# Performance work log

Measured on AMD Instinct MI355X. Metric: run time of the kernel, lower is better.

The kernel has to match this reference:

```python
import jax, jax.numpy as jnp
import numpy as np

LX = LY = KS = 14            # lengthX, lengthY, kernel_size
IN_BOND = 4
HID = 4                      # hidden_bond
CH = 2                       # channel
OUT = 10                     # output_dim
N = 32768                    # batch
LENGTH = LX * LY             # 196 sequential contraction steps
P = (LX - KS + 1) * (LY - KS + 1)  # number of patches (=1 here)
STD = 0.01
EPS = 1e-5                   # BatchNorm1d default eps


def setup_inputs() -> dict:
    key = jax.random.key(0)
    k0, k1, k2, k3 = jax.random.split(key, 4)
    x = jax.random.normal(k0, (N, IN_BOND, LX, LY), jnp.float32)
    # weights1[0]: [in_bond, hidden, channel]
    w_first = STD * jax.random.normal(k1, (IN_BOND, HID, CH), jnp.float32)
    # weights1[1..length-2]: [hidden, in_bond, hidden, channel], stacked
    w_mid = STD * jax.random.normal(k2, (LENGTH - 2, HID, IN_BOND, HID, CH), jnp.float32)
    # weights1[length-1]: [hidden, in_bond, output_dim, channel]
    w_last = STD * jax.random.normal(k3, (HID, IN_BOND, OUT, CH), jnp.float32)
    # shared BatchNorm1d(hidden) affine params
    gamma = jnp.ones((HID,), jnp.float32)
    beta = jnp.zeros((HID,), jnp.float32)
    return {"x": x, "w_first": w_first, "w_mid": w_mid, "w_last": w_last,
            "gamma": gamma, "beta": beta}


def reference(x, w_first, w_mid, w_last, gamma, beta):
    n = x.shape[0]
    # Patch extraction -> InputBucket [N, in_bond, KS*KS, P]
    buckets = []
    for k in range(LX - KS + 1):          # static, size 1 with defaults
        for l in range(LY - KS + 1):
            buckets.append(x[:, :, k:k + KS, l:l + KS].reshape(n, IN_BOND, KS * KS))
    ib = jnp.stack(buckets, axis=3)       # [N, in_bond, KS*KS, P]

    # Step 0: tensordot over in_bond, then permute -> y 'nbcr' = [N, P, CH, HID]
    y = jnp.einsum('nip,ihc->npch', ib[:, :, 0, :], w_first)

    # Middle steps 1..LENGTH-2 as a scan (strict sequential dependency chain)
    mids = jnp.moveaxis(ib[:, :, 1:LENGTH - 1, :], 2, 0)  # [LENGTH-2, N, in_bond, P]

    def step(y, inp):
        xi, w = inp  # xi: [N, in_bond, P]; w: [HID(r), IN_BOND(i), HID(h), CH(c)]
        # contra_w_d after permute: [N, P, CH, HID_left(r), HID_right(h)]
        contra = jnp.einsum('nip,rihc->npcrh', xi, w)
        y_new = jnp.einsum('npcr,npcrh->ncph', y, contra)  # 'ncbl': [N, CH, P, HID]
        # BatchNorm1d(HID) in training mode over flattened batch (biased var)
        flat = y_new.reshape(-1, HID)
        mean = jnp.mean(flat, axis=0)
        var = jnp.var(flat, axis=0)
        yb = (flat - mean) * jax.lax.rsqrt(var + EPS) * gamma + beta
        # faithful to torch's .view(-1, P, CH, HID) memory reinterpretation
        return yb.reshape(n, P, CH, HID), None

    y, _ = jax.lax.scan(step, y, (mids, w_mid))

    # Last step: -> [N, P, CH, HID, OUT] then einsum 'nbcr,nbcrl->nbcl'
    contra = jnp.einsum('nip,rioc->npcro', ib[:, :, LENGTH - 1, :], w_last)
    out = jnp.einsum('npcr,npcro->npco', y, contra)  # [N, P, CH, OUT]
    return out
```

## Files before the change

### kernel.cpp

```cpp
#include <hip/hip_runtime.h>

#define NSAMP 32768
#define INB   4
#define HIDN  4
#define CHN   2
#define OUTD  10
#define NPIX  196
#define NMID  194
#define BLK   256
#define SPT   2
#define NBLK  (NSAMP / (BLK * SPT))
#define INV_ROWS 1.52587890625e-05f
#define BN_EPS 1e-5f
#define SENT  0xFFFFFFFFFFFFFFFFull
#define WS_BYTES ((size_t)NMID * NBLK * 4 * sizeof(unsigned long long))

__device__ __forceinline__ float xcomp(const float4& v, int j) {
    return j == 0 ? v.x : j == 1 ? v.y : j == 2 ? v.z : v.w;
}

__device__ __forceinline__ void mid_step(
    int t, const float xv[SPT][INB], float y[SPT][CHN][HIDN],
    const float* __restrict__ wm,
    const float gm[HIDN], const float bt[HIDN],
    unsigned long long* __restrict__ slots,
    float (*pb)[8], float* totl, int tid)
{
    const float* w = wm + (long)t * (HIDN * INB * HIDN * CHN);
    float yn[SPT][CHN][HIDN];
#pragma unroll
    for (int s = 0; s < SPT; ++s)
#pragma unroll
        for (int c = 0; c < CHN; ++c)
#pragma unroll
            for (int h = 0; h < HIDN; ++h) yn[s][c][h] = 0.f;

#pragma unroll
    for (int s = 0; s < SPT; ++s)
#pragma unroll
        for (int r = 0; r < HIDN; ++r)
#pragma unroll
            for (int i = 0; i < INB; ++i) {
                float p0 = y[s][0][r] * xv[s][i];
                float p1 = y[s][1][r] * xv[s][i];
                const float* wri = w + r * (INB * HIDN * CHN) + i * (HIDN * CHN);
#pragma unroll
                for (int h = 0; h < HIDN; ++h) {
                    yn[s][0][h] = fmaf(p0, wri[h * CHN + 0], yn[s][0][h]);
                    yn[s][1][h] = fmaf(p1, wri[h * CHN + 1], yn[s][1][h]);
                }
            }
    float red[8];
#pragma unroll
    for (int h = 0; h < HIDN; ++h) {
        float sm = 0.f, sq = 0.f;
#pragma unroll
        for (int s = 0; s < SPT; ++s) {
            sm += yn[s][0][h] + yn[s][1][h];
            sq += yn[s][0][h] * yn[s][0][h] + yn[s][1][h] * yn[s][1][h];
        }
        red[h] = sm; red[4 + h] = sq;
    }
#pragma unroll
    for (int j = 0; j < 8; ++j)
#pragma unroll
        for (int off = 32; off > 0; off >>= 1)
            red[j] += __shfl_down(red[j], off);
    const int wv = tid >> 6, ln = tid & 63;
    if (ln == 0) {
#pragma unroll
        for (int j = 0; j < 8; ++j) pb[wv][j] = red[j];
    }
    __syncthreads();
    if (wv == 0) {
        if (ln < 4) {
            float lo = pb[0][2 * ln]     + pb[1][2 * ln]     + pb[2][2 * ln]     + pb[3][2 * ln];
            float hi = pb[0][2 * ln + 1] + pb[1][2 * ln + 1] + pb[2][2 * ln + 1] + pb[3][2 * ln + 1];
            unsigned long long v = ((unsigned long long)__float_as_uint(hi) << 32)
                                 |  (unsigned long long)__float_as_uint(lo);
            __hip_atomic_store(&slots[((size_t)t * NBLK + blockIdx.x) * 4 + ln], v,
                               __ATOMIC_RELAXED, __HIP_MEMORY_SCOPE_AGENT);
        }
        const unsigned long long* ps = &slots[((size_t)t * NBLK + ln) * 4];
        unsigned long long q0, q1, q2, q3;
        do {
            q0 = __hip_atomic_load(&ps[0], __ATOMIC_RELAXED, __HIP_MEMORY_SCOPE_AGENT);
            q1 = __hip_atomic_load(&ps[1], __ATOMIC_RELAXED, __HIP_MEMORY_SCOPE_AGENT);
            q2 = __hip_atomic_load(&ps[2], __ATOMIC_RELAXED, __HIP_MEMORY_SCOPE_AGENT);
            q3 = __hip_atomic_load(&ps[3], __ATOMIC_RELAXED, __HIP_MEMORY_SCOPE_AGENT);
        } while (!__all(q0 != SENT && q1 != SENT && q2 != SENT && q3 != SENT));
        float sm[8];
        sm[0] = __uint_as_float((unsigned)q0); sm[1] = __uint_as_float((unsigned)(q0 >> 32));
        sm[2] = __uint_as_float((unsigned)q1); sm[3] = __uint_as_float((unsigned)(q1 >> 32));
        sm[4] = __uint_as_float((unsigned)q2); sm[5] = __uint_as_float((unsigned)(q2 >> 32));
        sm[6] = __uint_as_float((unsigned)q3); sm[7] = __uint_as_float((unsigned)(q3 >> 32));
#pragma unroll
        for (int j = 0; j < 8; ++j)
#pragma unroll
            for (int off = 1; off < 64; off <<= 1)
                sm[j] += __shfl_xor(sm[j], off);
        if (ln < 8) totl[ln] = sm[ln];
    }
    __syncthreads();
    float sm[8];
#pragma unroll
    for (int j = 0; j < 8; ++j) sm[j] = totl[j];
#pragma unroll
    for (int h = 0; h < HIDN; ++h) {
        float m  = sm[h] * INV_ROWS;
        float v  = fmaf(-m, m, sm[4 + h] * INV_ROWS);
        float is = rsqrtf(v + BN_EPS) * gm[h];
        float sh = bt[h] - m * is;
#pragma unroll
        for (int s = 0; s < SPT; ++s) {
            y[s][0][h] = fmaf(yn[s][0][h], is, sh);
            y[s][1][h] = fmaf(yn[s][1][h], is, sh);
        }
    }
}

__global__ __launch_bounds__(BLK, 1)
void ttbn_main(const float* __restrict__ x,  const float* __restrict__ wf,
               const float* __restrict__ wm, const float* __restrict__ wl,
               const float* __restrict__ gamma, const float* __restrict__ beta,
               float* __restrict__ out, unsigned long long* __restrict__ slots)
{
    __shared__ float pb[BLK / 64][8];
    __shared__ float totl[8];
    const int tid = threadIdx.x;

    float gm[HIDN], bt[HIDN];
#pragma unroll
    for (int h = 0; h < HIDN; ++h) { gm[h] = gamma[h]; bt[h] = beta[h]; }

    const float* xn[SPT];
    long nidx[SPT];
#pragma unroll
    for (int s = 0; s < SPT; ++s) {
        nidx[s] = (long)blockIdx.x * (BLK * SPT) + s * BLK + tid;
        xn[s]   = x + nidx[s] * (INB * NPIX);
    }

    float4 xg[SPT][INB];
    float  y[SPT][CHN][HIDN];

#pragma unroll
    for (int s = 0; s < SPT; ++s)
#pragma unroll
        for (int i = 0; i < INB; ++i)
            xg[s][i] = *reinterpret_cast<const float4*>(xn[s] + i * NPIX);

#pragma unroll
    for (int s = 0; s < SPT; ++s)
#pragma unroll
        for (int c = 0; c < CHN; ++c)
#pragma unroll
            for (int h = 0; h < HIDN; ++h) {
                float acc = 0.f;
#pragma unroll
                for (int i = 0; i < INB; ++i)
                    acc = fmaf(xg[s][i].x, wf[i * (HIDN * CHN) + h * CHN + c], acc);
                y[s][c][h] = acc;
            }
#pragma unroll
    for (int slp = 1; slp < 4; ++slp) {
        float xv[SPT][INB];
#pragma unroll
        for (int s = 0; s < SPT; ++s)
#pragma unroll
            for (int i = 0; i < INB; ++i) xv[s][i] = xcomp(xg[s][i], slp);
        mid_step(slp - 1, xv, y, wm, gm, bt, slots, pb, totl, tid);
    }

#pragma unroll 1
    for (int g = 1; g < 48; ++g) {
#pragma unroll
        for (int s = 0; s < SPT; ++s)
#pragma unroll
            for (int i = 0; i < INB; ++i)
                xg[s][i] = *reinterpret_cast<const float4*>(xn[s] + i * NPIX + g * 4);
#pragma unroll
        for (int slp = 0; slp < 4; ++slp) {
            float xv[SPT][INB];
#pragma unroll
            for (int s = 0; s < SPT; ++s)
#pragma unroll
                for (int i = 0; i < INB; ++i) xv[s][i] = xcomp(xg[s][i], slp);
            mid_step(g * 4 + slp - 1, xv, y, wm, gm, bt, slots, pb, totl, tid);
        }
    }

#pragma unroll
    for (int s = 0; s < SPT; ++s)
#pragma unroll
        for (int i = 0; i < INB; ++i)
            xg[s][i] = *reinterpret_cast<const float4*>(xn[s] + i * NPIX + 192);
#pragma unroll
    for (int slp = 0; slp < 3; ++slp) {
        float xv[SPT][INB];
#pragma unroll
        for (int s = 0; s < SPT; ++s)
#pragma unroll
            for (int i = 0; i < INB; ++i) xv[s][i] = xcomp(xg[s][i], slp);
        mid_step(191 + slp, xv, y, wm, gm, bt, slots, pb, totl, tid);
    }
#pragma unroll
    for (int s = 0; s < SPT; ++s) {
        float xv[INB];
#pragma unroll
        for (int i = 0; i < INB; ++i) xv[i] = xg[s][i].w;
        float o0[OUTD], o1[OUTD];
#pragma unroll
        for (int od = 0; od < OUTD; ++od) { o0[od] = 0.f; o1[od] = 0.f; }
#pragma unroll
        for (int r = 0; r < 4; ++r)
#pragma unroll
            for (int i = 0; i < INB; ++i) {
                float p0 = y[s][0][r] * xv[i];
                float p1 = y[s][1][r] * xv[i];
                const float* wri = wl + r * (INB * OUTD * CHN) + i * (OUTD * CHN);
#pragma unroll
                for (int od = 0; od < OUTD; ++od) {
                    o0[od] = fmaf(p0, wri[od * CHN + 0], o0[od]);
                    o1[od] = fmaf(p1, wri[od * CHN + 1], o1[od]);
                }
            }
        float tmp[20];
#pragma unroll
        for (int od = 0; od < OUTD; ++od) { tmp[od] = o0[od]; tmp[10 + od] = o1[od]; }
        float4* o4 = reinterpret_cast<float4*>(out + nidx[s] * (CHN * OUTD));
#pragma unroll
        for (int q = 0; q < 5; ++q)
            o4[q] = make_float4(tmp[q * 4], tmp[q * 4 + 1], tmp[q * 4 + 2], tmp[q * 4 + 3]);
    }
}

extern "C" void kernel_launch(void* const* d_in, const int* in_sizes, int n_in,
                              void* d_out, int out_size, void* d_ws, size_t ws_size,
                              hipStream_t stream) {
    const float* x     = (const float*)d_in[0];
    const float* wf    = (const float*)d_in[1];
    const float* wm    = (const float*)d_in[2];
    const float* wl    = (const float*)d_in[3];
    const float* gamma = (const float*)d_in[4];
    const float* beta  = (const float*)d_in[5];
    float*       out   = (float*)d_out;
    unsigned long long* slots = (unsigned long long*)d_ws;

    hipMemsetAsync(d_ws, 0xFF, WS_BYTES, stream);

    void* args[] = { &x, &wf, &wm, &wl, &gamma, &beta, &out, &slots };
    hipLaunchCooperativeKernel((void*)ttbn_main, dim3(NBLK), dim3(BLK),
                               args, 0, stream);
}
```

Measured before the change: 848.7 us.

## Halve block count, simplify grid-wide BN reduction, prefetch inputs in float2 pairs

Doubles samples per thread so the grid has half as many blocks (32 instead of 64), which shrinks the cross-block slot polling in each of the 194 grid-wide BatchNorm barriers to two loads per lane and a shorter shuffle tree. Input loading changes from float4 groups of four steps to float2 pairs, with the next pair software-prefetched one iteration ahead. The cost is more register pressure from four samples per thread and fewer active CUs doing the per-step math.

```diff
diff --git a/kernel.cpp b/kernel.cpp
--- a/kernel.cpp
+++ b/kernel.cpp
@@ -8,16 +8,12 @@
 #define NPIX  196
 #define NMID  194
 #define BLK   256
-#define SPT   2
+#define SPT   4
 #define NBLK  (NSAMP / (BLK * SPT))
 #define INV_ROWS 1.52587890625e-05f
 #define BN_EPS 1e-5f
 #define SENT  0xFFFFFFFFFFFFFFFFull
 #define WS_BYTES ((size_t)NMID * NBLK * 4 * sizeof(unsigned long long))
-
-__device__ __forceinline__ float xcomp(const float4& v, int j) {
-    return j == 0 ? v.x : j == 1 ? v.y : j == 2 ? v.z : v.w;
-}
 
 __device__ __forceinline__ void mid_step(
     int t, const float xv[SPT][INB], float y[SPT][CHN][HIDN],
@@ -26,7 +22,7 @@
     unsigned long long* __restrict__ slots,
     float (*pb)[8], float* totl, int tid)
 {
-    const float* w = wm + (long)t * (HIDN * INB * HIDN * CHN);
+    const float* w = wm + (long)t * 128;
     float yn[SPT][CHN][HIDN];
 #pragma unroll
     for (int s = 0; s < SPT; ++s)
@@ -81,25 +77,20 @@
             __hip_atomic_store(&slots[((size_t)t * NBLK + blockIdx.x) * 4 + ln], v,
                                __ATOMIC_RELAXED, __HIP_MEMORY_SCOPE_AGENT);
         }
-        const unsigned long long* ps = &slots[((size_t)t * NBLK + ln) * 4];
-        unsigned long long q0, q1, q2, q3;
+        const unsigned long long* base = slots + (size_t)t * NBLK * 4;
+        unsigned long long q0, q1;
         do {
-            q0 = __hip_atomic_load(&ps[0], __ATOMIC_RELAXED, __HIP_MEMORY_SCOPE_AGENT);
-            q1 = __hip_atomic_load(&ps[1], __ATOMIC_RELAXED, __HIP_MEMORY_SCOPE_AGENT);
-            q2 = __hip_atomic_load(&ps[2], __ATOMIC_RELAXED, __HIP_MEMORY_SCOPE_AGENT);
-            q3 = __hip_atomic_load(&ps[3], __ATOMIC_RELAXED, __HIP_MEMORY_SCOPE_AGENT);
-        } while (!__all(q0 != SENT && q1 != SENT && q2 != SENT && q3 != SENT));
-        float sm[8];
-        sm[0] = __uint_as_float((unsigned)q0); sm[1] = __uint_as_float((unsigned)(q0 >> 32));
-        sm[2] = __uint_as_float((unsigned)q1); sm[3] = __uint_as_float((unsigned)(q1 >> 32));
-        sm[4] = __uint_as_float((unsigned)q2); sm[5] = __uint_as_float((unsigned)(q2 >> 32));
-        sm[6] = __uint_as_float((unsigned)q3); sm[7] = __uint_as_float((unsigned)(q3 >> 32));
-#pragma unroll
-        for (int j = 0; j < 8; ++j)
-#pragma unroll
-            for (int off = 1; off < 64; off <<= 1)
-                sm[j] += __shfl_xor(sm[j], off);
-        if (ln < 8) totl[ln] = sm[ln];
+            q0 = __hip_atomic_load(base + ln,      __ATOMIC_RELAXED, __HIP_MEMORY_SCOPE_AGENT);
+            q1 = __hip_atomic_load(base + ln + 64, __ATOMIC_RELAXED, __HIP_MEMORY_SCOPE_AGENT);
+        } while (!__all(q0 != SENT && q1 != SENT));
+        float slo = __uint_as_float((unsigned)q0) + __uint_as_float((unsigned)q1);
+        float shi = __uint_as_float((unsigned)(q0 >> 32)) + __uint_as_float((unsigned)(q1 >> 32));
+#pragma unroll
+        for (int d = 4; d < 64; d <<= 1) {
+            slo += __shfl_xor(slo, d);
+            shi += __shfl_xor(shi, d);
+        }
+        if (ln < 4) { totl[2 * ln] = slo; totl[2 * ln + 1] = shi; }
     }
     __syncthreads();
     float sm[8];
@@ -141,14 +132,14 @@
         xn[s]   = x + nidx[s] * (INB * NPIX);
     }
 
-    float4 xg[SPT][INB];
+    float2 xg[SPT][INB], xg2[SPT][INB];
     float  y[SPT][CHN][HIDN];
 
 #pragma unroll
     for (int s = 0; s < SPT; ++s)
 #pragma unroll
         for (int i = 0; i < INB; ++i)
-            xg[s][i] = *reinterpret_cast<const float4*>(xn[s] + i * NPIX);
+            xg[s][i] = *reinterpret_cast<const float2*>(xn[s] + i * NPIX);
 
 #pragma unroll
     for (int s = 0; s < SPT; ++s)
@@ -163,57 +154,70 @@
                 y[s][c][h] = acc;
             }
 #pragma unroll
-    for (int slp = 1; slp < 4; ++slp) {
+    for (int s = 0; s < SPT; ++s)
+#pragma unroll
+        for (int i = 0; i < INB; ++i)
+            xg2[s][i] = *reinterpret_cast<const float2*>(xn[s] + i * NPIX + 2);
+    {
         float xv[SPT][INB];
 #pragma unroll
         for (int s = 0; s < SPT; ++s)
 #pragma unroll
-            for (int i = 0; i < INB; ++i) xv[s][i] = xcomp(xg[s][i], slp);
-        mid_step(slp - 1, xv, y, wm, gm, bt, slots, pb, totl, tid);
+            for (int i = 0; i < INB; ++i) xv[s][i] = xg[s][i].y;
+        mid_step(0, xv, y, wm, gm, bt, slots, pb, totl, tid);
     }
 
 #pragma unroll 1
-    for (int g = 1; g < 48; ++g) {
+    for (int g = 1; g < 97; ++g) {
+#pragma unroll
+        for (int s = 0; s < SPT; ++s)
+#pragma unroll
+            for (int i = 0; i < INB; ++i) xg[s][i] = xg2[s][i];
 #pragma unroll
         for (int s = 0; s < SPT; ++s)
 #pragma unroll
             for (int i = 0; i < INB; ++i)
-                xg[s][i] = *reinterpret_cast<const float4*>(xn[s] + i * NPIX + g * 4);
-#pragma unroll
-        for (int slp = 0; slp < 4; ++slp) {
+                xg2[s][i] = *reinterpret_cast<const float2*>(xn[s] + i * NPIX + 2 * (g + 1));
+        {
             float xv[SPT][INB];
 #pragma unroll
             for (int s = 0; s < SPT; ++s)
 #pragma unroll
-                for (int i = 0; i < INB; ++i) xv[s][i] = xcomp(xg[s][i], slp);
-            mid_step(g * 4 + slp - 1, xv, y, wm, gm, bt, slots, pb, totl, tid);
-        }
-    }
-
-#pragma unroll
-    for (int s = 0; s < SPT; ++s)
-#pragma unroll
-        for (int i = 0; i < INB; ++i)
-            xg[s][i] = *reinterpret_cast<const float4*>(xn[s] + i * NPIX + 192);
-#pragma unroll
-    for (int slp = 0; slp < 3; ++slp) {
+                for (int i = 0; i < INB; ++i) xv[s][i] = xg[s][i].x;
+            mid_step(2 * g - 1, xv, y, wm, gm, bt, slots, pb, totl, tid);
+        }
+        {
+            float xv[SPT][INB];
+#pragma unroll
+            for (int s = 0; s < SPT; ++s)
+#pragma unroll
+                for (int i = 0; i < INB; ++i) xv[s][i] = xg[s][i].y;
+            mid_step(2 * g, xv, y, wm, gm, bt, slots, pb, totl, tid);
+        }
+    }
+
+#pragma unroll
+    for (int s = 0; s < SPT; ++s)
+#pragma unroll
+        for (int i = 0; i < INB; ++i) xg[s][i] = xg2[s][i];
+    {
         float xv[SPT][INB];
 #pragma unroll
         for (int s = 0; s < SPT; ++s)
 #pragma unroll
-            for (int i = 0; i < INB; ++i) xv[s][i] = xcomp(xg[s][i], slp);
-        mid_step(191 + slp, xv, y, wm, gm, bt, slots, pb, totl, tid);
+            for (int i = 0; i < INB; ++i) xv[s][i] = xg[s][i].x;
+        mid_step(193, xv, y, wm, gm, bt, slots, pb, totl, tid);
     }
 #pragma unroll
     for (int s = 0; s < SPT; ++s) {
         float xv[INB];
 #pragma unroll
-        for (int i = 0; i < INB; ++i) xv[i] = xg[s][i].w;
+        for (int i = 0; i < INB; ++i) xv[i] = xg[s][i].y;
         float o0[OUTD], o1[OUTD];
 #pragma unroll
         for (int od = 0; od < OUTD; ++od) { o0[od] = 0.f; o1[od] = 0.f; }
 #pragma unroll
-        for (int r = 0; r < 4; ++r)
+        for (int r = 0; r < HIDN; ++r)
 #pragma unroll
             for (int i = 0; i < INB; ++i) {
                 float p0 = y[s][0][r] * xv[i];
```

Measured after the change: 1.101 ms. 29.7% more time.
